# Performance work log

Measured on AMD Instinct MI355X. Metric: run time of the kernel, lower is better.

Reference implementation:

```python
import jax, jax.numpy as jnp
import numpy as np

NUM_GROUPS = 8
EPS = 1e-6

def group_norm(x, gamma, beta):
    # x: [B, C, L]
    B, C, L = x.shape
    g = x.reshape(B, NUM_GROUPS, (C // NUM_GROUPS) * L)
    mean = g.mean(axis=-1, keepdims=True)
    var = g.var(axis=-1, keepdims=True)
    g = (g - mean) * jax.lax.rsqrt(var + EPS)
    g = g.reshape(B, C, L)
    return g * gamma[None, :, None] + beta[None, :, None]

def conv1x1(h, w, b):
    # w: [O, C], b: [O]; h: [B, C, L]
    return jnp.einsum('oc,bcl->bol', w, h) + b[None, :, None]

def setup_inputs() -> dict:
    key = jax.random.key(0)
    ks = jax.random.split(key, 12)
    B, C, L = 8, 512, 2048
    s = 1.0 / np.sqrt(C)
    inp = {
        'x': jax.random.normal(ks[0], (B, C, L), dtype=jnp.float32),
        'gamma': jnp.ones((C,), jnp.float32),
        'beta': jnp.zeros((C,), jnp.float32),
        'wq': jax.random.uniform(ks[1], (C, C), jnp.float32, -s, s),
        'bq': jax.random.uniform(ks[2], (C,), jnp.float32, -s, s),
        'wk': jax.random.uniform(ks[3], (C, C), jnp.float32, -s, s),
        'bk': jax.random.uniform(ks[4], (C,), jnp.float32, -s, s),
        'wv': jax.random.uniform(ks[5], (C, C), jnp.float32, -s, s),
        'bv': jax.random.uniform(ks[6], (C,), jnp.float32, -s, s),
        'wo': jax.random.uniform(ks[7], (C, C), jnp.float32, -s, s),
        'bo': jax.random.uniform(ks[8], (C,), jnp.float32, -s, s),
    }
    return inp

def reference(x, gamma, beta, wq, bq, wk, bk, wv, bv, wo, bo):
    C = x.shape[1]
    h = group_norm(x, gamma, beta)
    q = conv1x1(h, wq, bq)  # [B, C, L]
    k = conv1x1(h, wk, bk)
    v = conv1x1(h, wv, bv)
    # scores: [B, Lq, Lk] = q^T k, scaled by C^-0.5
    w = jnp.einsum('bci,bcj->bij', q, k) * (C ** -0.5)
    w = jax.nn.softmax(w, axis=2)
    # h[b,c,i] = sum_j v[b,c,j] * w[b,i,j]
    h = jnp.einsum('bcj,bij->bci', v, w)
    h = conv1x1(h, wo, bo)
    return x + h
```

## Files before the change

kernel.cpp:

```cpp
#include <hip/hip_runtime.h>
#include <hip/hip_bf16.h>
#include <cstdio>

typedef __attribute__((ext_vector_type(8))) short short8;
typedef __attribute__((ext_vector_type(8))) unsigned short ushort8;
typedef __attribute__((ext_vector_type(4))) float f32x4;
typedef __attribute__((ext_vector_type(4))) unsigned short ushort4v;

__device__ inline unsigned short f2bf(float f){
    unsigned int u = __float_as_uint(f);
    unsigned int r = (u + 0x7fffu + ((u >> 16) & 1u)) >> 16;
    return (unsigned short)r;
}
__device__ inline float bf2f(unsigned short b){
    return __uint_as_float((unsigned int)b << 16);
}

__device__ inline void store1(float* p, float v){ *p = v; }
__device__ inline void store1(unsigned short* p, float v){ *p = f2bf(v); }

#define BM 128
#define BN 128

template<typename OutT, int EPI>
__global__ __launch_bounds__(256)
void gemm_nt(const unsigned short* __restrict__ Ag,
             const unsigned short* __restrict__ Bg,
             OutT* __restrict__ Cg,
             int K, int lda, int ldb, int ldc,
             long sA, long sB, long sC,
             const float* __restrict__ bias,
             const float* __restrict__ resid, long sR,
             float scale)
{
    const int gx = gridDim.x, gy = gridDim.y;
    const int nwg  = gx * gy * (int)gridDim.z;
    const int orig = blockIdx.x + gx * (blockIdx.y + gy * blockIdx.z);
    const int cpx  = nwg >> 3;
    const int nid  = (orig & 7) * cpx + (orig >> 3);
    const int bx   = nid % gx;
    const int tmp  = nid / gx;
    const int by   = tmp % gy;
    const int bz   = tmp / gy;

    Ag += (long)bz * sA;
    Bg += (long)bz * sB;
    Cg += (long)bz * sC;
    const int m0 = by * BM;
    const int n0 = bx * BN;

    __shared__ unsigned short As[2][128 * 64];
    __shared__ unsigned short Bs[2][128 * 64];

    const int t    = threadIdx.x;
    const int wave = t >> 6;
    const int lane = t & 63;
    const int wm   = (wave >> 1) << 6;
    const int wn   = (wave & 1) << 6;
    const int lhi  = lane >> 4;
    const int llo  = lane & 15;

    f32x4 acc[4][4];
#pragma unroll
    for (int i = 0; i < 4; i++)
#pragma unroll
        for (int j = 0; j < 4; j++) acc[i][j] = (f32x4)(0.0f);

    auto stage = [&](int bi, int k0){
#pragma unroll
        for (int i = 0; i < 4; i++){
            const int tt = i * 256 + t;
            const int r  = tt >> 3;
            const int cb = tt & 7;
            const int cs = cb ^ (r & 7);
            const unsigned short* gpA = Ag + (long)(m0 + r) * lda + k0 + cs * 8;
            const unsigned short* gpB = Bg + (long)(n0 + r) * ldb + k0 + cs * 8;
            unsigned short* lpA = &As[bi][i * 2048 + wave * 512];
            unsigned short* lpB = &Bs[bi][i * 2048 + wave * 512];
            __builtin_amdgcn_global_load_lds(
                (const __attribute__((address_space(1))) void*)gpA,
                (__attribute__((address_space(3))) void*)lpA, 16, 0, 0);
            __builtin_amdgcn_global_load_lds(
                (const __attribute__((address_space(1))) void*)gpB,
                (__attribute__((address_space(3))) void*)lpB, 16, 0, 0);
        }
    };

    const int nt = K >> 6;
    stage(0, 0);
    __syncthreads();

    int cur = 0;
    for (int kt = 0; kt < nt; kt++){
        if (kt + 1 < nt) stage(cur ^ 1, (kt + 1) << 6);
#pragma unroll
        for (int ksub = 0; ksub < 2; ksub++){
            short8 af[4], bf[4];
#pragma unroll
            for (int mi = 0; mi < 4; mi++){
                const int r  = wm + mi * 16 + llo;
                const int cs = (ksub * 4 + lhi) ^ (r & 7);
                af[mi] = *(const short8*)(&As[cur][r * 64 + cs * 8]);
            }
#pragma unroll
            for (int ni = 0; ni < 4; ni++){
                const int r  = wn + ni * 16 + llo;
                const int cs = (ksub * 4 + lhi) ^ (r & 7);
                bf[ni] = *(const short8*)(&Bs[cur][r * 64 + cs * 8]);
            }
#pragma unroll
            for (int mi = 0; mi < 4; mi++)
#pragma unroll
                for (int ni = 0; ni < 4; ni++)
                    acc[mi][ni] = __builtin_amdgcn_mfma_f32_16x16x32_bf16(
                        af[mi], bf[ni], acc[mi][ni], 0, 0, 0);
        }
        __syncthreads();
        cur ^= 1;
    }

#pragma unroll
    for (int mi = 0; mi < 4; mi++){
#pragma unroll
        for (int ni = 0; ni < 4; ni++){
            const int n  = n0 + wn + ni * 16 + llo;
            const int mb = m0 + wm + mi * 16 + lhi * 4;
            f32x4 v = acc[mi][ni];
#pragma unroll
            for (int j = 0; j < 4; j++){
                const int m = mb + j;
                float val = v[j] * scale;
                if (EPI == 1) val += bias[n];
                if (EPI == 2) val += bias[m];
                if (EPI == 3) val += bias[m] + resid[(long)bz * sR + (long)m * ldc + n];
                store1(&Cg[(long)m * ldc + n], val);
            }
        }
    }
}


__global__ void gn_partial(const float* __restrict__ x, float* __restrict__ part){
    const long base = (long)blockIdx.x * 8192;
    const float4* xp = (const float4*)(x + base);
    float s = 0.f, ss = 0.f;
    for (int i = threadIdx.x; i < 2048; i += 256){
        float4 v = xp[i];
        s  += (v.x + v.y) + (v.z + v.w);
        ss += (v.x * v.x + v.y * v.y) + (v.z * v.z + v.w * v.w);
    }
    for (int o = 32; o; o >>= 1){ s += __shfl_down(s, o); ss += __shfl_down(ss, o); }
    __shared__ float rs[4], rss[4];
    const int wave = threadIdx.x >> 6, lane = threadIdx.x & 63;
    if (lane == 0){ rs[wave] = s; rss[wave] = ss; }
    __syncthreads();
    if (threadIdx.x == 0){
        part[blockIdx.x * 2]     = (rs[0] + rs[1]) + (rs[2] + rs[3]);
        part[blockIdx.x * 2 + 1] = (rss[0] + rss[1]) + (rss[2] + rss[3]);
    }
}

__global__ void gn_final(const float* __restrict__ part, float* __restrict__ stats){
    const int bg = threadIdx.x;
    if (bg >= 64) return;
    float s = 0.f, ss = 0.f;
    for (int c = 0; c < 16; c++){
        s  += part[(bg * 16 + c) * 2];
        ss += part[(bg * 16 + c) * 2 + 1];
    }
    const float inv_n = 1.0f / 131072.0f;
    const float mean = s * inv_n;
    const float var  = ss * inv_n - mean * mean;
    stats[bg * 2]     = mean;
    stats[bg * 2 + 1] = rsqrtf(var + 1e-6f);
}

__global__ void norm_transpose(const float* __restrict__ x, const float* __restrict__ stats,
                               const float* __restrict__ gamma, const float* __restrict__ beta,
                               unsigned short* __restrict__ ht){
    const int b = blockIdx.z, c0 = blockIdx.y * 64, l0 = blockIdx.x * 64;
    const int bg = b * 8 + (c0 >> 6);
    const float mean = stats[bg * 2], rstd = stats[bg * 2 + 1];
    __shared__ unsigned short tile[64][66];
    const float* xb = x + (long)b * 1048576;
    const int t = threadIdx.x;
#pragma unroll
    for (int i = 0; i < 16; i++){
        const int idx = i * 256 + t;
        const int c = idx >> 6, l = idx & 63;
        float v = xb[(long)(c0 + c) * 2048 + l0 + l];
        v = (v - mean) * rstd * gamma[c0 + c] + beta[c0 + c];
        tile[l][c] = f2bf(v);
    }
    __syncthreads();
    unsigned short* htb = ht + (long)b * 1048576;
#pragma unroll
    for (int i = 0; i < 16; i++){
        const int idx = i * 256 + t;
        const int l = idx >> 6, c = idx & 63;
        htb[(long)(l0 + l) * 512 + c0 + c] = tile[l][c];
    }
}

__global__ void weights_to_bf16(const float4* __restrict__ wq, const float4* __restrict__ wk,
                                const float4* __restrict__ wv, const float4* __restrict__ wo,
                                ushort4v* __restrict__ out){
    const int i = blockIdx.x * 256 + threadIdx.x;
    const int w = i >> 16, off = i & 65535;
    const float4* src = (w == 0) ? wq : (w == 1) ? wk : (w == 2) ? wv : wo;
    float4 v = src[off];
    ushort4v o;
    o.x = f2bf(v.x); o.y = f2bf(v.y); o.z = f2bf(v.z); o.w = f2bf(v.w);
    out[i] = o;
}

__global__ void softmax_inplace(unsigned short* __restrict__ p){
    const long base = (long)blockIdx.x * 2048;
    ushort8* pp = (ushort8*)(p + base);
    const int t = threadIdx.x;
    ushort8 v = pp[t];
    float f[8];
#pragma unroll
    for (int j = 0; j < 8; j++) f[j] = bf2f(v[j]);
    float mx = f[0];
#pragma unroll
    for (int j = 1; j < 8; j++) mx = fmaxf(mx, f[j]);
    for (int o = 32; o; o >>= 1) mx = fmaxf(mx, __shfl_xor(mx, o));
    __shared__ float rmax[4], rsum[4];
    const int wave = t >> 6, lane = t & 63;
    if (lane == 0) rmax[wave] = mx;
    __syncthreads();
    mx = fmaxf(fmaxf(rmax[0], rmax[1]), fmaxf(rmax[2], rmax[3]));
    float sum = 0.f;
#pragma unroll
    for (int j = 0; j < 8; j++){ f[j] = __expf(f[j] - mx); sum += f[j]; }
    for (int o = 32; o; o >>= 1) sum += __shfl_xor(sum, o);
    if (lane == 0) rsum[wave] = sum;
    __syncthreads();
    sum = (rsum[0] + rsum[1]) + (rsum[2] + rsum[3]);
    const float inv = 1.0f / sum;
    ushort8 o8;
#pragma unroll
    for (int j = 0; j < 8; j++) o8[j] = f2bf(f[j] * inv);
    pp[t] = o8;
}

enum : long {
    OFF_WQ  = 0,
    OFF_WK  = 524288,
    OFF_WV  = 1048576,
    OFF_WO  = 1572864,
    OFF_HT  = 2097152,
    OFF_QT  = OFF_HT  + 16777216,
    OFF_KT  = OFF_QT  + 16777216,
    OFF_V   = OFF_KT  + 16777216,
    OFF_H2  = OFF_V   + 16777216,
    OFF_P   = OFF_H2  + 16777216,
    OFF_GNP = OFF_P   + 67108864,
    OFF_GNS = OFF_GNP + 8192,
    OFF_END = OFF_GNS + 512
};

extern "C" void kernel_launch(void* const* d_in, const int* in_sizes, int n_in,
                              void* d_out, int out_size, void* d_ws, size_t ws_size,
                              hipStream_t stream)
{
    const float* x     = (const float*)d_in[0];
    const float* gamma = (const float*)d_in[1];
    const float* beta  = (const float*)d_in[2];
    const float* wq    = (const float*)d_in[3];
    const float* bq    = (const float*)d_in[4];
    const float* wk    = (const float*)d_in[5];
    const float* bk    = (const float*)d_in[6];
    const float* wv    = (const float*)d_in[7];
    const float* bv    = (const float*)d_in[8];
    const float* wo    = (const float*)d_in[9];
    const float* bo    = (const float*)d_in[10];
    float* out = (float*)d_out;
    char* ws = (char*)d_ws;

    if (ws_size < (size_t)OFF_END){
        fprintf(stderr, "kernel_launch: ws too small (%zu < %ld)\n", ws_size, (long)OFF_END);
        return;
    }

    unsigned short* HT  = (unsigned short*)(ws + OFF_HT);
    unsigned short* QT  = (unsigned short*)(ws + OFF_QT);
    unsigned short* KT  = (unsigned short*)(ws + OFF_KT);
    unsigned short* V   = (unsigned short*)(ws + OFF_V);
    unsigned short* H2  = (unsigned short*)(ws + OFF_H2);
    unsigned short* P   = (unsigned short*)(ws + OFF_P);
    float*          GNP = (float*)(ws + OFF_GNP);
    float*          GNS = (float*)(ws + OFF_GNS);
    unsigned short* WQb = (unsigned short*)(ws + OFF_WQ);
    unsigned short* WKb = (unsigned short*)(ws + OFF_WK);
    unsigned short* WVb = (unsigned short*)(ws + OFF_WV);
    unsigned short* WOb = (unsigned short*)(ws + OFF_WO);

    const long LC = 1048576;
    const long LL = 4194304;

    weights_to_bf16<<<1024, 256, 0, stream>>>(
        (const float4*)wq, (const float4*)wk, (const float4*)wv, (const float4*)wo,
        (ushort4v*)(ws + OFF_WQ));

    gn_partial<<<1024, 256, 0, stream>>>(x, GNP);
    gn_final<<<1, 64, 0, stream>>>(GNP, GNS);
    norm_transpose<<<dim3(32, 8, 8), 256, 0, stream>>>(x, GNS, gamma, beta, HT);

    gemm_nt<unsigned short, 1><<<dim3(4, 16, 8), 256, 0, stream>>>(
        HT, WQb, QT, 512, 512, 512, 512, LC, 0, LC, bq, nullptr, 0, 1.0f);
    gemm_nt<unsigned short, 1><<<dim3(4, 16, 8), 256, 0, stream>>>(
        HT, WKb, KT, 512, 512, 512, 512, LC, 0, LC, bk, nullptr, 0, 1.0f);
    gemm_nt<unsigned short, 2><<<dim3(16, 4, 8), 256, 0, stream>>>(
        WVb, HT, V, 512, 512, 512, 2048, 0, LC, LC, bv, nullptr, 0, 1.0f);

    gemm_nt<unsigned short, 0><<<dim3(16, 16, 8), 256, 0, stream>>>(
        QT, KT, P, 512, 512, 512, 2048, LC, LC, LL, nullptr, nullptr, 0, 0.04419417382f);

    softmax_inplace<<<16384, 256, 0, stream>>>(P);

    gemm_nt<unsigned short, 0><<<dim3(4, 16, 8), 256, 0, stream>>>(
        P, V, H2, 2048, 2048, 2048, 512, LL, LC, LC, nullptr, nullptr, 0, 1.0f);

    gemm_nt<float, 3><<<dim3(16, 4, 8), 256, 0, stream>>>(
        WOb, H2, out, 512, 512, 512, 2048, 0, LC, LC, bo, x, LC, 1.0f);
}
```

Measured before the change: 285.8 us.

## Add 256x256-tile 8-wave GEMM with interleaved staging for attention matmuls

Adds a new GEMM kernel with 256x256 output tiles, 512 threads (8 waves, each owning a 128x64 subtile), and double-buffered global-to-LDS loads. The next tile's loads are spread across four compute phases, with explicit vmcnt waits, barriers and setprio. The kernel is used for the QK^T score GEMM and the PV GEMM, which are the largest matmuls. The goal is more data reuse per LDS byte and better overlap of loads with MFMA work. The cost is 128 KB of LDS per block and heavy register use, which limits occupancy. The PV GEMM also gets only 128 workgroups.

```diff
diff --git a/kernel.cpp b/kernel.cpp
--- a/kernel.cpp
+++ b/kernel.cpp
@@ -19,8 +19,149 @@
 __device__ inline void store1(float* p, float v){ *p = v; }
 __device__ inline void store1(unsigned short* p, float v){ *p = f2bf(v); }
 
-#define BM 128
-#define BN 128
+#define GLDS(gp, lp) __builtin_amdgcn_global_load_lds( \
+    (const __attribute__((address_space(1))) void*)(gp), \
+    (__attribute__((address_space(3))) void*)(lp), 16, 0, 0)
+
+#define WAITV(N) asm volatile("s_waitcnt vmcnt(" #N ")" ::: "memory")
+
+template<typename OutT, int EPI>
+__global__ __launch_bounds__(512, 2)
+void gemm256(const unsigned short* __restrict__ Ag,
+             const unsigned short* __restrict__ Bg,
+             OutT* __restrict__ Cg,
+             int K, int lda, int ldb, int ldc,
+             long sA, long sB, long sC,
+             const float* __restrict__ bias,
+             const float* __restrict__ resid, long sR,
+             float scale)
+{
+    const int gx = gridDim.x, gy = gridDim.y;
+    const int nwg  = gx * gy * (int)gridDim.z;
+    const int orig = blockIdx.x + gx * (blockIdx.y + gy * blockIdx.z);
+    const int cpx  = nwg >> 3;
+    const int nid  = (orig & 7) * cpx + (orig >> 3);
+    const int bx   = nid % gx;
+    const int tmp  = nid / gx;
+    const int by   = tmp % gy;
+    const int bz   = tmp / gy;
+
+    Ag += (long)bz * sA;
+    Bg += (long)bz * sB;
+    Cg += (long)bz * sC;
+    const int m0 = by * 256;
+    const int n0 = bx * 256;
+
+    __shared__ unsigned short As[2][16384];
+    __shared__ unsigned short Bs[2][16384];
+
+    const int t    = threadIdx.x;
+    const int wave = t >> 6;
+    const int lane = t & 63;
+    const int rg   = wave >> 2;
+    const int cg   = wave & 3;
+    const int wm   = rg * 128;
+    const int wn   = cg * 64;
+    const int lhi  = lane >> 4;
+    const int llo  = lane & 15;
+
+    f32x4 acc[4][8];
+#pragma unroll
+    for (int p = 0; p < 4; p++)
+#pragma unroll
+        for (int f = 0; f < 8; f++) acc[p][f] = (f32x4)(0.0f);
+
+    const int s_rr = t >> 3, s_cb = t & 7;
+    const int s_cs = s_cb ^ (s_rr & 7);
+    auto stageA = [&](int bi, int k0, int j){
+        GLDS(Ag + (long)(m0 + j * 64 + s_rr) * lda + k0 + s_cs * 8,
+             &As[bi][j * 4096 + wave * 512]);
+    };
+    auto stageB = [&](int bi, int k0, int j){
+        GLDS(Bg + (long)(n0 + j * 64 + s_rr) * ldb + k0 + s_cs * 8,
+             &Bs[bi][j * 4096 + wave * 512]);
+    };
+
+    const int nt = K >> 6;
+    stageB(0, 0, 0); stageB(0, 0, 1); stageB(0, 0, 2); stageB(0, 0, 3);
+    stageA(0, 0, 0); stageA(0, 0, 2); stageA(0, 0, 1); stageA(0, 0, 3);
+    WAITV(2);
+    __builtin_amdgcn_s_barrier();
+    __builtin_amdgcn_sched_barrier(0);
+
+    int cur = 0;
+    for (int kt = 0; kt < nt; kt++){
+        const bool more = (kt + 1 < nt);
+        const int nk0 = (kt + 1) << 6;
+#pragma unroll
+        for (int p = 0; p < 4; p++){
+            const int h = p >> 1, cl = p & 1;
+            short8 af[2][4], bf[2][2];
+#pragma unroll
+            for (int ks = 0; ks < 2; ks++){
+#pragma unroll
+                for (int mi = 0; mi < 4; mi++){
+                    const int r  = wm + h * 64 + mi * 16 + llo;
+                    const int pc = (ks * 4 + lhi) ^ (r & 7);
+                    af[ks][mi] = *(const short8*)(&As[cur][r * 64 + pc * 8]);
+                }
+#pragma unroll
+                for (int ni = 0; ni < 2; ni++){
+                    const int r  = wn + cl * 32 + ni * 16 + llo;
+                    const int pc = (ks * 4 + lhi) ^ (r & 7);
+                    bf[ks][ni] = *(const short8*)(&Bs[cur][r * 64 + pc * 8]);
+                }
+            }
+            __builtin_amdgcn_sched_barrier(0);
+            if (more){
+                if (p == 0){ stageB(cur ^ 1, nk0, 0); stageB(cur ^ 1, nk0, 1); }
+                if (p == 1){ stageB(cur ^ 1, nk0, 2); stageB(cur ^ 1, nk0, 3); }
+                if (p == 2){ stageA(cur ^ 1, nk0, 0); stageA(cur ^ 1, nk0, 2); }
+                if (p == 3){ stageA(cur ^ 1, nk0, 1); stageA(cur ^ 1, nk0, 3); }
+            }
+            if (p == 1){ if (more) WAITV(4); else WAITV(0); }
+            if (p == 3){ if (more) WAITV(2); }
+            __builtin_amdgcn_s_barrier();
+            __builtin_amdgcn_sched_barrier(0);
+            __builtin_amdgcn_s_setprio(1);
+#pragma unroll
+            for (int ks = 0; ks < 2; ks++)
+#pragma unroll
+                for (int mi = 0; mi < 4; mi++)
+#pragma unroll
+                    for (int ni = 0; ni < 2; ni++)
+                        acc[p][mi * 2 + ni] = __builtin_amdgcn_mfma_f32_16x16x32_bf16(
+                            af[ks][mi], bf[ks][ni], acc[p][mi * 2 + ni], 0, 0, 0);
+            __builtin_amdgcn_s_setprio(0);
+            __builtin_amdgcn_s_barrier();
+            __builtin_amdgcn_sched_barrier(0);
+        }
+        cur ^= 1;
+    }
+
+#pragma unroll
+    for (int p = 0; p < 4; p++){
+        const int h = p >> 1, cl = p & 1;
+#pragma unroll
+        for (int mi = 0; mi < 4; mi++){
+#pragma unroll
+            for (int ni = 0; ni < 2; ni++){
+                const int n  = n0 + wn + cl * 32 + ni * 16 + llo;
+                const int mb = m0 + wm + h * 64 + mi * 16 + lhi * 4;
+                f32x4 v = acc[p][mi * 2 + ni];
+#pragma unroll
+                for (int j = 0; j < 4; j++){
+                    const int m = mb + j;
+                    float val = v[j] * scale;
+                    if (EPI == 1) val += bias[n];
+                    if (EPI == 2) val += bias[m];
+                    if (EPI == 3) val += bias[m] + resid[(long)bz * sR + (long)m * ldc + n];
+                    store1(&Cg[(long)m * ldc + n], val);
+                }
+            }
+        }
+    }
+}
 
 template<typename OutT, int EPI>
 __global__ __launch_bounds__(256)
@@ -46,8 +187,8 @@
     Ag += (long)bz * sA;
     Bg += (long)bz * sB;
     Cg += (long)bz * sC;
-    const int m0 = by * BM;
-    const int n0 = bx * BN;
+    const int m0 = by * 128;
+    const int n0 = bx * 128;
 
     __shared__ unsigned short As[2][128 * 64];
     __shared__ unsigned short Bs[2][128 * 64];
@@ -73,16 +214,8 @@
             const int r  = tt >> 3;
             const int cb = tt & 7;
             const int cs = cb ^ (r & 7);
-            const unsigned short* gpA = Ag + (long)(m0 + r) * lda + k0 + cs * 8;
-            const unsigned short* gpB = Bg + (long)(n0 + r) * ldb + k0 + cs * 8;
-            unsigned short* lpA = &As[bi][i * 2048 + wave * 512];
-            unsigned short* lpB = &Bs[bi][i * 2048 + wave * 512];
-            __builtin_amdgcn_global_load_lds(
-                (const __attribute__((address_space(1))) void*)gpA,
-                (__attribute__((address_space(3))) void*)lpA, 16, 0, 0);
-            __builtin_amdgcn_global_load_lds(
-                (const __attribute__((address_space(1))) void*)gpB,
-                (__attribute__((address_space(3))) void*)lpB, 16, 0, 0);
+            GLDS(Ag + (long)(m0 + r) * lda + k0 + cs * 8, &As[bi][i * 2048 + wave * 512]);
+            GLDS(Bg + (long)(n0 + r) * ldb + k0 + cs * 8, &Bs[bi][i * 2048 + wave * 512]);
         }
     };
 
@@ -315,12 +448,12 @@
     gemm_nt<unsigned short, 2><<<dim3(16, 4, 8), 256, 0, stream>>>(
         WVb, HT, V, 512, 512, 512, 2048, 0, LC, LC, bv, nullptr, 0, 1.0f);
 
-    gemm_nt<unsigned short, 0><<<dim3(16, 16, 8), 256, 0, stream>>>(
+    gemm256<unsigned short, 0><<<dim3(8, 8, 8), 512, 0, stream>>>(
         QT, KT, P, 512, 512, 512, 2048, LC, LC, LL, nullptr, nullptr, 0, 0.04419417382f);
 
     softmax_inplace<<<16384, 256, 0, stream>>>(P);
 
-    gemm_nt<unsigned short, 0><<<dim3(4, 16, 8), 256, 0, stream>>>(
+    gemm256<unsigned short, 0><<<dim3(2, 8, 8), 512, 0, stream>>>(
         P, V, H2, 2048, 2048, 2048, 512, LL, LC, LC, nullptr, nullptr, 0, 1.0f);
 
     gemm_nt<float, 3><<<dim3(16, 4, 8), 256, 0, stream>>>(
```

Result: slower. 309.0 us (+8.1%).
